# Kernel tuning notes

Hardware: AMD Instinct MI355X
Metric: run time of the kernel (lower is better)

## Reference

```python
import jax, jax.numpy as jnp
import numpy as np
from jax import lax

DIM = 256
HEADS = 8
DIM_HEAD = 32
INNER = HEADS * DIM_HEAD  # 256
FF_MULT = 4
FFI = DIM * FF_MULT       # 1024
TOP_H = 16
TOP_W = 16
EPS_LN = 1e-5
EPS_IN = 1e-5


def conv1x1(x, w, b=None):
    # x: (b,c,h,w), w: (o,c)
    y = jnp.einsum('oc,bchw->bohw', w, x)
    if b is not None:
        y = y + b[None, :, None, None]
    return y


def dwconv3x3(x, w, b):
    # x: (b,c,h,w), w: (c,1,3,3) depthwise
    c = x.shape[1]
    y = lax.conv_general_dilated(x, w, window_strides=(1, 1), padding='SAME',
                                 feature_group_count=c,
                                 dimension_numbers=('NCHW', 'OIHW', 'NCHW'))
    return y + b[None, :, None, None]


def chan_layernorm(x, g, b):
    mean = jnp.mean(x, axis=1, keepdims=True)
    var = jnp.var(x, axis=1, keepdims=True)  # biased, matches unbiased=False
    return (x - mean) / jnp.sqrt(var + EPS_LN) * g + b


def instnorm(x):
    # InstanceNorm2d(affine=False): normalize per (b,c) over spatial dims
    mean = jnp.mean(x, axis=(2, 3), keepdims=True)
    var = jnp.var(x, axis=(2, 3), keepdims=True)
    return (x - mean) / jnp.sqrt(var + EPS_IN)


def l2norm_lastdim(t):
    # F.normalize(t, dim=-1): normalize along the LAST axis (width here)
    n = jnp.sqrt(jnp.sum(t * t, axis=-1, keepdims=True))
    return t / jnp.maximum(n, 1e-12)


def dpsa(x, ln_g, ln_b, w_qkv, w_out, b_out):
    b, c, H, W = x.shape
    xn = chan_layernorm(x, ln_g, ln_b)
    qkv = conv1x1(xn, w_qkv)                       # (b, 3*INNER, H, W)
    q, k, v = jnp.split(qkv, 3, axis=1)
    # fold heads: 'b (h c) x y -> (b h) c x y'
    fold = lambda t: t.reshape(b, HEADS, DIM_HEAD, H, W).reshape(b * HEADS, DIM_HEAD, H, W)
    q, k, v = fold(q), fold(k), fold(v)
    q = l2norm_lastdim(q)
    k = l2norm_lastdim(k)

    B = b * HEADS
    q_probe = jnp.sum(q, axis=(2, 3))              # (B, c)

    # height pruning
    k_height = jnp.sum(k, axis=3)                  # (B, c, H)
    score_r = jnp.einsum('bc,bch->bh', q_probe, k_height)
    _, top_h = lax.top_k(score_r, TOP_H)           # (B, TOP_H)
    idx_h = top_h[:, None, :, None]
    k = jnp.take_along_axis(k, idx_h, axis=2)      # (B, c, TOP_H, W)
    v = jnp.take_along_axis(v, idx_h, axis=2)

    # width pruning
    k_width = jnp.sum(k, axis=2)                   # (B, c, W)
    score_c = jnp.einsum('bc,bcw->bw', q_probe, k_width)
    _, top_w = lax.top_k(score_c, TOP_W)           # (B, TOP_W)
    idx_w = top_w[:, None, None, :]
    k = jnp.take_along_axis(k, idx_w, axis=3)      # (B, c, TOP_H, TOP_W)
    v = jnp.take_along_axis(v, idx_w, axis=3)

    # 'b d h w -> b (h w) d'
    flat = lambda t: t.transpose(0, 2, 3, 1).reshape(B, -1, DIM_HEAD)
    qf, kf, vf = flat(q), flat(k), flat(v)
    sim = jnp.einsum('bid,bjd->bij', qf, kf)       # (B, HW, TOP_H*TOP_W) — no scale, matches source
    attn = jax.nn.softmax(sim, axis=-1)
    out = jnp.einsum('bij,bjd->bid', attn, vf)     # (B, HW, d)
    # '(b h) (x y) d -> b (h d) x y'
    out = out.reshape(b, HEADS, H, W, DIM_HEAD).transpose(0, 1, 4, 2, 3).reshape(b, INNER, H, W)
    return conv1x1(out, w_out, b_out)


def setup_inputs() -> dict:
    key = jax.random.key(0)
    ks = jax.random.split(key, 12)
    s = 0.02
    return {
        'x': jax.random.normal(ks[0], (8, DIM, 64, 64), dtype=jnp.float32),
        'ln_g': jnp.ones((1, DIM, 1, 1), jnp.float32),
        'ln_b': jnp.zeros((1, DIM, 1, 1), jnp.float32),
        'w_qkv': jax.random.normal(ks[1], (3 * INNER, DIM), jnp.float32) * s,
        'w_out': jax.random.normal(ks[2], (DIM, INNER), jnp.float32) * s,
        'b_out': jnp.zeros((DIM,), jnp.float32),
        'w_dw': jax.random.normal(ks[3], (DIM, 1, 3, 3), jnp.float32) * s,
        'b_dw': jnp.zeros((DIM,), jnp.float32),
        'w_comb': jax.random.normal(ks[4], (DIM, 2 * DIM), jnp.float32) * s,
        'b_comb': jnp.zeros((DIM,), jnp.float32),
        'w_ff1': jax.random.normal(ks[5], (FFI, DIM), jnp.float32) * s,
        'b_ff1': jnp.zeros((FFI,), jnp.float32),
        'w_ffdw': jax.random.normal(ks[6], (FFI, 1, 3, 3), jnp.float32) * s,
        'b_ffdw': jnp.zeros((FFI,), jnp.float32),
        'w_ff2': jax.random.normal(ks[7], (DIM, FFI), jnp.float32) * s,
        'b_ff2': jnp.zeros((DIM,), jnp.float32),
    }


def reference(x, ln_g, ln_b, w_qkv, w_out, b_out, w_dw, b_dw, w_comb, b_comb,
              w_ff1, b_ff1, w_ffdw, b_ffdw, w_ff2, b_ff2):
    attn_branch = dpsa(x, ln_g, ln_b, w_qkv, w_out, b_out)
    conv_branch = dwconv3x3(x, w_dw, b_dw)
    combined = jnp.concatenate([attn_branch, conv_branch], axis=1)
    attn_out = conv1x1(combined, w_comb, b_comb) + x
    # feed-forward
    h = conv1x1(attn_out, w_ff1, b_ff1)
    h = jax.nn.gelu(instnorm(h), approximate=False)
    r = jax.nn.gelu(instnorm(dwconv3x3(h, w_ffdw, b_ffdw)), approximate=False)
    h = h + r
    h = conv1x1(h, w_ff2, b_ff2)
    return instnorm(h)
```

## Files before the change

### kernel.cpp

```cpp
#include <hip/hip_runtime.h>
#include <math.h>

constexpr int Bn = 8, Cd = 256, HW = 4096;
constexpr int NPOS = Bn * HW;

typedef __attribute__((ext_vector_type(8))) short bfrag;
typedef __attribute__((ext_vector_type(4))) float facc;
typedef __attribute__((ext_vector_type(8))) unsigned short us8;

static __device__ __forceinline__ float wredsum(float v){
  #pragma unroll
  for (int d=32; d; d>>=1) v += __shfl_xor(v,d,64);
  return v;
}
static __device__ __forceinline__ float gelu_exact(float x){
  return 0.5f*x*(1.f+erff(x*0.70710678118f));
}
static __device__ __forceinline__ unsigned short bf16r(float x){
  unsigned u = __float_as_uint(x);
  u += 0x7FFFu + ((u>>16)&1u);
  return (unsigned short)(u>>16);
}
static __device__ __forceinline__ void split1(float x, unsigned short& h, unsigned short& l){
  unsigned u = __float_as_uint(x);
  unsigned r = (u + 0x7FFFu + ((u>>16)&1u)) & 0xFFFF0000u;
  h = (unsigned short)(r>>16);
  float rest = x - __uint_as_float(r);
  unsigned u2 = __float_as_uint(rest);
  unsigned r2 = u2 + 0x7FFFu + ((u2>>16)&1u);
  l = (unsigned short)(r2>>16);
}

__global__ __launch_bounds__(256) void k_lnsplit(const float* __restrict__ x,
    const float* __restrict__ g, const float* __restrict__ bb,
    unsigned short* __restrict__ xt){
  __shared__ float rs[64][5], rss[64][5];
  int pxi = threadIdx.x & 63;
  int cg  = threadIdx.x >> 6;
  int p = blockIdx.x*64 + pxi;
  int b = p >> 12, pos = p & 4095;
  const float* xb = x + ((size_t)b*Cd + cg*64)*(size_t)HW + pos;
  float s=0.f, ss=0.f;
  #pragma unroll 8
  for (int c=0;c<64;c++){ float v = xb[(size_t)c*HW]; s+=v; ss+=v*v; }
  rs[pxi][cg]=s; rss[pxi][cg]=ss;
  __syncthreads();
  s  = rs[pxi][0]+rs[pxi][1]+rs[pxi][2]+rs[pxi][3];
  ss = rss[pxi][0]+rss[pxi][1]+rss[pxi][2]+rss[pxi][3];
  float mean = s*(1.f/Cd);
  float inv  = rsqrtf(ss*(1.f/Cd) - mean*mean + 1e-5f);
  unsigned short* xh = xt + (size_t)b*2097152ull + (size_t)pos*256u + cg*64;
  unsigned short* xl = xh + 1048576u;
  for (int c0=0;c0<64;c0+=8){
    us8 hv, lv;
    #pragma unroll
    for (int j=0;j<8;j++){
      float v = xb[(size_t)(c0+j)*HW];
      v = (v-mean)*inv*g[cg*64+c0+j] + bb[cg*64+c0+j];
      unsigned short hh,ll; split1(v,hh,ll);
      hv[j]=hh; lv[j]=ll;
    }
    *(us8*)(xh + c0) = hv;
    *(us8*)(xl + c0) = lv;
  }
}

__global__ void k_splitW(const float* __restrict__ w, unsigned short* __restrict__ wh, int n){
  int i = blockIdx.x*256 + threadIdx.x;
  if (i<n){
    unsigned short h,l; split1(w[i],h,l);
    wh[i]=h; wh[n+i]=l;
  }
}
__global__ void k_cvtW(const float* __restrict__ w, unsigned short* __restrict__ wb, int n){
  int i = blockIdx.x*256 + threadIdx.x;
  if (i<n) wb[i] = bf16r(w[i]);
}

__global__ __launch_bounds__(256) void k_mfma3(
    const unsigned short* __restrict__ W2,
    const unsigned short* __restrict__ Xt,
    float* __restrict__ out, int M, int K, long xbs){
  int b  = blockIdx.z;
  int n0 = blockIdx.x*128;
  int m0 = blockIdx.y*128;
  int wave = threadIdx.x>>6, lane = threadIdx.x&63;
  int wm = (wave>>1)*64, wn = (wave&1)*64;
  int l15 = lane&15, half = lane>>4;
  const unsigned short* Wh = W2;
  const unsigned short* Wl = W2 + (size_t)M*K;
  const unsigned short* Xh = Xt + (size_t)b*(size_t)xbs;
  const unsigned short* Xl = Xh + (size_t)4096u*(size_t)K;

  facc acc[4][4];
  #pragma unroll
  for (int i=0;i<4;i++)
    #pragma unroll
    for (int j=0;j<4;j++) acc[i][j] = (facc){0.f,0.f,0.f,0.f};

  const size_t wrow[4] = {
    (size_t)(m0+wm+ 0+l15)*(size_t)K, (size_t)(m0+wm+16+l15)*(size_t)K,
    (size_t)(m0+wm+32+l15)*(size_t)K, (size_t)(m0+wm+48+l15)*(size_t)K };
  const size_t xrow[4] = {
    (size_t)(n0+wn+ 0+l15)*(size_t)K, (size_t)(n0+wn+16+l15)*(size_t)K,
    (size_t)(n0+wn+32+l15)*(size_t)K, (size_t)(n0+wn+48+l15)*(size_t)K };

  for (int k0=0; k0<K; k0+=32){
    int ks = k0 + half*8;
    bfrag ah[4], al[4], bh[4], bl[4];
    #pragma unroll
    for (int i=0;i<4;i++){
      ah[i] = *(const bfrag*)(Wh + wrow[i] + ks);
      al[i] = *(const bfrag*)(Wl + wrow[i] + ks);
      bh[i] = *(const bfrag*)(Xh + xrow[i] + ks);
      bl[i] = *(const bfrag*)(Xl + xrow[i] + ks);
    }
    #pragma unroll
    for (int i=0;i<4;i++)
      #pragma unroll
      for (int j=0;j<4;j++){
        acc[i][j] = __builtin_amdgcn_mfma_f32_16x16x32_bf16(ah[i], bh[j], acc[i][j],0,0,0);
        acc[i][j] = __builtin_amdgcn_mfma_f32_16x16x32_bf16(ah[i], bl[j], acc[i][j],0,0,0);
        acc[i][j] = __builtin_amdgcn_mfma_f32_16x16x32_bf16(al[i], bh[j], acc[i][j],0,0,0);
      }
  }
  #pragma unroll
  for (int i=0;i<4;i++){
    int o = m0+wm+i*16+half*4;
    #pragma unroll
    for (int j=0;j<4;j++){
      int p = n0+wn+j*16+l15;
      size_t ob = ((size_t)b*M + o)*(size_t)HW + p;
      #pragma unroll
      for (int r=0;r<4;r++)
        out[ob + (size_t)r*HW] = acc[i][j][r];
    }
  }
}

template<bool RES>
__global__ __launch_bounds__(256) void k_mfma1(
    const unsigned short* __restrict__ Wb,
    const unsigned short* __restrict__ Xt,
    const float* __restrict__ bias, const float* __restrict__ resid,
    float* __restrict__ out, int M, int K, long xbs){
  int b  = blockIdx.z;
  int n0 = blockIdx.x*128;
  int m0 = blockIdx.y*128;
  int wave = threadIdx.x>>6, lane = threadIdx.x&63;
  int wm = (wave>>1)*64, wn = (wave&1)*64;
  int l15 = lane&15, half = lane>>4;
  const unsigned short* Xh = Xt + (size_t)b*(size_t)xbs;

  facc acc[4][4];
  #pragma unroll
  for (int i=0;i<4;i++)
    #pragma unroll
    for (int j=0;j<4;j++) acc[i][j] = (facc){0.f,0.f,0.f,0.f};

  const size_t wrow[4] = {
    (size_t)(m0+wm+ 0+l15)*(size_t)K, (size_t)(m0+wm+16+l15)*(size_t)K,
    (size_t)(m0+wm+32+l15)*(size_t)K, (size_t)(m0+wm+48+l15)*(size_t)K };
  const size_t xrow[4] = {
    (size_t)(n0+wn+ 0+l15)*(size_t)K, (size_t)(n0+wn+16+l15)*(size_t)K,
    (size_t)(n0+wn+32+l15)*(size_t)K, (size_t)(n0+wn+48+l15)*(size_t)K };

  #pragma unroll 2
  for (int k0=0; k0<K; k0+=32){
    int ks = k0 + half*8;
    bfrag ah[4], bh[4];
    #pragma unroll
    for (int i=0;i<4;i++){
      ah[i] = *(const bfrag*)(Wb + wrow[i] + ks);
      bh[i] = *(const bfrag*)(Xh + xrow[i] + ks);
    }
    #pragma unroll
    for (int i=0;i<4;i++)
      #pragma unroll
      for (int j=0;j<4;j++)
        acc[i][j] = __builtin_amdgcn_mfma_f32_16x16x32_bf16(ah[i], bh[j], acc[i][j],0,0,0);
  }
  #pragma unroll
  for (int i=0;i<4;i++){
    int o = m0+wm+i*16+half*4;
    #pragma unroll
    for (int j=0;j<4;j++){
      int p = n0+wn+j*16+l15;
      size_t ob = ((size_t)b*M + o)*(size_t)HW + p;
      #pragma unroll
      for (int r=0;r<4;r++){
        float v = acc[i][j][r];
        if (bias) v += bias[o+r];
        if (RES)  v += resid[ob + (size_t)r*HW];
        out[ob + (size_t)r*HW] = v;
      }
    }
  }
}

__global__ __launch_bounds__(256) void k_l2norm(float* __restrict__ qkv,
    float* __restrict__ k_height){
  int row  = blockIdx.x*4 + (threadIdx.x>>6);
  int lane = threadIdx.x & 63;
  int part = row >> 17;
  int rem  = row & 131071;
  int Bp   = rem >> 11;
  int c    = (rem >> 6) & 31;
  int h    = rem & 63;
  int b = Bp>>3, hd = Bp&7;
  float* ptr = qkv + ((size_t)b*768 + part*256 + hd*32 + c)*(size_t)HW + h*64;
  float v = ptr[lane];
  float ss = v*v, sv = v;
  #pragma unroll
  for (int d=32; d; d>>=1){ ss += __shfl_xor(ss,d,64); sv += __shfl_xor(sv,d,64); }
  float inv = 1.f / fmaxf(sqrtf(ss), 1e-12f);
  ptr[lane] = v*inv;
  if (lane==0 && part) k_height[(size_t)Bp*2048 + c*64 + h] = sv*inv;
}

__global__ __launch_bounds__(256) void k_qT(const float* __restrict__ qkv,
    unsigned short* __restrict__ qt){
  __shared__ float t[64][33];
  int Bp = blockIdx.y, p0 = blockIdx.x*64;
  int b = Bp>>3, hd = Bp&7;
  const float* qp = qkv + ((size_t)b*768 + hd*32)*(size_t)HW + p0;
  int c8 = threadIdx.x>>6, px = threadIdx.x&63;
  #pragma unroll
  for (int j=0;j<8;j++)
    t[px][c8*8+j] = qp[(size_t)(c8*8+j)*HW + px];
  __syncthreads();
  int px2 = threadIdx.x>>2, ch = threadIdx.x&3;
  us8 hv;
  #pragma unroll
  for (int j=0;j<8;j++) hv[j] = bf16r(t[px2][ch*8+j]);
  *(us8*)(qt + ((size_t)Bp*4096 + p0 + px2)*32 + ch*8) = hv;
}

__global__ __launch_bounds__(256) void k_qprobe(const float* __restrict__ qkv,
    float* __restrict__ q_probe){
  int Bp = blockIdx.x >> 5;
  int c  = blockIdx.x & 31;
  int b = Bp>>3, hd = Bp&7;
  const float* qp = qkv + ((size_t)b*768 + hd*32 + c)*(size_t)HW;
  float s = 0.f;
  for (int i=threadIdx.x*4; i<HW; i+=1024){
    float4 v = *(const float4*)(qp+i);
    s += v.x+v.y+v.z+v.w;
  }
  s = wredsum(s);
  __shared__ float red[4];
  if ((threadIdx.x&63)==0) red[threadIdx.x>>6] = s;
  __syncthreads();
  if (threadIdx.x==0) q_probe[blockIdx.x] = red[0]+red[1]+red[2]+red[3];
}

__global__ void k_score(const float* __restrict__ q_probe,
    const float* __restrict__ agg, float* __restrict__ score){
  int Bp = blockIdx.x; int t = threadIdx.x;
  float s = 0.f;
  for (int c=0;c<32;c++) s += q_probe[Bp*32+c] * agg[(size_t)Bp*2048 + c*64 + t];
  score[Bp*64+t] = s;
}

__global__ void k_topk(const float* __restrict__ score, int* __restrict__ idx){
  int Bp = blockIdx.x; int lane = threadIdx.x;
  float v = score[Bp*64+lane];
  for (int it=0; it<16; ++it){
    float m = v;
    #pragma unroll
    for (int d=32; d; d>>=1) m = fmaxf(m, __shfl_xor(m,d,64));
    unsigned long long mask = __ballot(v==m);
    int sel = __ffsll((unsigned long long)mask) - 1;
    if (lane==0) idx[Bp*16+it] = sel;
    if (lane==sel) v = -3.0e38f;
  }
}

__global__ void k_kwidth(const float* __restrict__ qkv, const int* __restrict__ idx_h,
    float* __restrict__ k_width){
  int c = blockIdx.x, Bp = blockIdx.y, w = threadIdx.x;
  int b = Bp>>3, hd = Bp&7;
  const float* kp = qkv + ((size_t)b*768 + 256 + hd*32 + c)*(size_t)HW;
  float s = 0.f;
  for (int i=0;i<16;i++) s += kp[idx_h[Bp*16+i]*64 + w];
  k_width[(size_t)Bp*2048 + c*64 + w] = s;
}

__global__ __launch_bounds__(256) void k_gather_bf(const float* __restrict__ qkv,
    const int* __restrict__ idx_h, const int* __restrict__ idx_w,
    unsigned short* __restrict__ kfb, unsigned short* __restrict__ vtb){
  int Bp = blockIdx.x; int b = Bp>>3, hd = Bp&7;
  __shared__ int hi[16], wj[16];
  __shared__ int pos_s[256];
  if (threadIdx.x < 16) hi[threadIdx.x] = idx_h[Bp*16+threadIdx.x];
  else if (threadIdx.x < 32) wj[threadIdx.x-16] = idx_w[Bp*16+threadIdx.x-16];
  __syncthreads();
  pos_s[threadIdx.x] = hi[threadIdx.x>>4]*64 + wj[threadIdx.x&15];
  __syncthreads();
  const float* kpl = qkv + ((size_t)b*768 + 256 + hd*32)*(size_t)HW;
  const float* vpl = qkv + ((size_t)b*768 + 512 + hd*32)*(size_t)HW;
  for (int e=threadIdx.x; e<8192; e+=256){
    int t = e>>5, c = e&31;
    kfb[(size_t)Bp*8192 + e] = bf16r(kpl[(size_t)c*HW + pos_s[t]]);
    int c2 = e>>8, t2 = e&255;
    vtb[(size_t)Bp*8192 + e] = bf16r(vpl[(size_t)c2*HW + pos_s[t2]]);
  }
}

__global__ __launch_bounds__(256) void k_attn_mfma(
    const unsigned short* __restrict__ QT,
    const unsigned short* __restrict__ kfb,
    const unsigned short* __restrict__ vtb,
    unsigned short* __restrict__ xout){
  __shared__ unsigned short Pl[4*16*264];
  __shared__ unsigned short obuf[4*16*32];
  __shared__ float lsum[64];
  int Bp = blockIdx.y, qb = blockIdx.x*64;
  int b = Bp>>3, hd = Bp&7;
  int tid = threadIdx.x;
  int wv = tid>>6, lane = tid&63, l15 = lane&15, lq = lane>>4;

  const unsigned short* Kg = kfb + (size_t)Bp*8192;
  const unsigned short* Vg = vtb + (size_t)Bp*8192;

  bfrag aq = *(const bfrag*)(QT + ((size_t)Bp*4096 + qb + wv*16 + l15)*32 + lq*8);

  float ps[4] = {0.f,0.f,0.f,0.f};
  #pragma unroll
  for (int t=0;t<16;t++){
    bfrag bk = *(const bfrag*)(Kg + (t*16+l15)*32 + lq*8);
    facc s = (facc){0.f,0.f,0.f,0.f};
    s = __builtin_amdgcn_mfma_f32_16x16x32_bf16(aq, bk, s, 0,0,0);
    #pragma unroll
    for (int r=0;r<4;r++){
      float pe = __expf(s[r]);
      ps[r] += pe;
      Pl[(wv*16 + lq*4 + r)*264 + t*16 + l15] = bf16r(pe);
    }
  }
  #pragma unroll
  for (int r=0;r<4;r++){
    #pragma unroll
    for (int d=1; d<16; d<<=1) ps[r] += __shfl_xor(ps[r], d, 64);
  }
  if (l15==0){
    #pragma unroll
    for (int r=0;r<4;r++) lsum[wv*16 + lq*4 + r] = ps[r];
  }

  facc o0 = (facc){0.f,0.f,0.f,0.f}, o1 = (facc){0.f,0.f,0.f,0.f};
  #pragma unroll
  for (int ko=0;ko<8;ko++){
    bfrag ap = *(const bfrag*)(Pl + (wv*16 + l15)*264 + ko*32 + lq*8);
    bfrag b0 = *(const bfrag*)(Vg + (l15)*256 + ko*32 + lq*8);
    bfrag b1 = *(const bfrag*)(Vg + (16+l15)*256 + ko*32 + lq*8);
    o0 = __builtin_amdgcn_mfma_f32_16x16x32_bf16(ap, b0, o0, 0,0,0);
    o1 = __builtin_amdgcn_mfma_f32_16x16x32_bf16(ap, b1, o1, 0,0,0);
  }
  #pragma unroll
  for (int r=0;r<4;r++){
    float iv = 1.f / lsum[wv*16 + lq*4 + r];
    obuf[(wv*16 + lq*4 + r)*32 + l15]      = bf16r(o0[r]*iv);
    obuf[(wv*16 + lq*4 + r)*32 + 16 + l15] = bf16r(o1[r]*iv);
  }
  int ql = wv*16 + (lane>>2), ch = lane&3;
  us8 hv = *(const us8*)(obuf + ql*32 + ch*8);
  *(us8*)(xout + (size_t)b*6291456ull + (size_t)(qb + ql)*256u + hd*32 + ch*8) = hv;
}

__global__ __launch_bounds__(256) void k_bf16T(const float* __restrict__ in,
    unsigned short* __restrict__ xt, int Cpart, int Ktot, int coff, int rb0, int wb0){
  int rb = rb0 + blockIdx.z, wb = wb0 + blockIdx.z;
  int c0 = blockIdx.y*64, p0 = blockIdx.x*64;
  __shared__ float t[64][65];
  const float* ip = in + ((size_t)rb*Cpart + c0)*(size_t)HW + p0;
  int tr = threadIdx.x>>4, tc4 = (threadIdx.x&15)*4;
  #pragma unroll
  for (int rr=0; rr<64; rr+=16){
    float4 v = *(const float4*)(ip + (size_t)(tr+rr)*HW + tc4);
    t[tr+rr][tc4+0]=v.x; t[tr+rr][tc4+1]=v.y; t[tr+rr][tc4+2]=v.z; t[tr+rr][tc4+3]=v.w;
  }
  __syncthreads();
  unsigned short* xh = xt + (size_t)wb*4096u*(size_t)Ktot + (size_t)coff + c0;
  #pragma unroll
  for (int rr=0; rr<64; rr+=16){
    int p = tr+rr;
    ushort4 hv;
    hv.x = bf16r(t[tc4+0][p]); hv.y = bf16r(t[tc4+1][p]);
    hv.z = bf16r(t[tc4+2][p]); hv.w = bf16r(t[tc4+3][p]);
    *(ushort4*)(xh + (size_t)(p0+p)*(size_t)Ktot + tc4) = hv;
  }
}

__global__ __launch_bounds__(256) void k_dwbf16(const float* __restrict__ x,
    const float* __restrict__ w, const float* __restrict__ bias,
    unsigned short* __restrict__ xt){
  int p = blockIdx.x*256 + threadIdx.x;
  int b = p >> 12, pos = p & 4095;
  int h = pos>>6, wx = pos&63;
  int c0 = blockIdx.y*64;
  unsigned short* xh = xt + (size_t)b*2097152ull + (size_t)pos*512u + 256u + c0;
  for (int cc=0; cc<64; cc+=8){
    us8 hv;
    #pragma unroll
    for (int j=0;j<8;j++){
      int c = c0+cc+j;
      const float* ip = x + ((size_t)b*Cd + c)*(size_t)HW;
      const float* wp = w + c*9;
      float s = bias[c];
      #pragma unroll
      for (int kh=-1; kh<=1; ++kh){
        int hh = h+kh; if ((unsigned)hh >= 64u) continue;
        #pragma unroll
        for (int kw=-1; kw<=1; ++kw){
          int ww2 = wx+kw; if ((unsigned)ww2 >= 64u) continue;
          s += wp[(kh+1)*3 + (kw+1)] * ip[hh*64 + ww2];
        }
      }
      hv[j] = bf16r(s);
    }
    *(us8*)(xh+cc) = hv;
  }
}

__global__ __launch_bounds__(256) void k_ffn_fused(float* __restrict__ h,
    const float* __restrict__ wdw, const float* __restrict__ bdw){
  __shared__ float lds[4096];
  __shared__ float red[8];
  int plane = blockIdx.x;
  int c = plane & 1023;
  float* hp = h + (size_t)plane*(size_t)HW;
  int t = threadIdx.x;
  int wid = t>>6, lane = t&63;

  float4 v[4];
  float s=0.f, ss=0.f;
  #pragma unroll
  for (int k2=0;k2<4;k2++){
    v[k2] = *(const float4*)(hp + k2*1024 + t*4);
    s  += v[k2].x+v[k2].y+v[k2].z+v[k2].w;
    ss += v[k2].x*v[k2].x+v[k2].y*v[k2].y+v[k2].z*v[k2].z+v[k2].w*v[k2].w;
  }
  s = wredsum(s); ss = wredsum(ss);
  if (lane==0){ red[wid]=s; red[4+wid]=ss; }
  __syncthreads();
  s  = red[0]+red[1]+red[2]+red[3];
  ss = red[4]+red[5]+red[6]+red[7];
  float mean = s*(1.f/HW);
  float inv  = rsqrtf(ss*(1.f/HW) - mean*mean + 1e-5f);

  #pragma unroll
  for (int k2=0;k2<4;k2++){
    int i = k2*1024 + t*4;
    lds[i+0] = gelu_exact((v[k2].x-mean)*inv);
    lds[i+1] = gelu_exact((v[k2].y-mean)*inv);
    lds[i+2] = gelu_exact((v[k2].z-mean)*inv);
    lds[i+3] = gelu_exact((v[k2].w-mean)*inv);
  }
  __syncthreads();

  float w9[9];
  #pragma unroll
  for (int i=0;i<9;i++) w9[i] = wdw[c*9+i];
  float bv = bdw[c];
  float r[16];
  float s2=0.f, ss2=0.f;
  #pragma unroll
  for (int k2=0;k2<4;k2++){
    #pragma unroll
    for (int j=0;j<4;j++){
      int px = k2*1024 + t*4 + j;
      int hh = px>>6, ww = px&63;
      float acc = bv;
      #pragma unroll
      for (int kh=-1; kh<=1; ++kh){
        int h2 = hh+kh; if ((unsigned)h2 >= 64u) continue;
        #pragma unroll
        for (int kw=-1; kw<=1; ++kw){
          int w2 = ww+kw; if ((unsigned)w2 >= 64u) continue;
          acc += w9[(kh+1)*3+(kw+1)] * lds[h2*64 + w2];
        }
      }
      r[k2*4+j] = acc;
      s2 += acc; ss2 += acc*acc;
    }
  }
  s2 = wredsum(s2); ss2 = wredsum(ss2);
  __syncthreads();
  if (lane==0){ red[wid]=s2; red[4+wid]=ss2; }
  __syncthreads();
  s2  = red[0]+red[1]+red[2]+red[3];
  ss2 = red[4]+red[5]+red[6]+red[7];
  float mean2 = s2*(1.f/HW);
  float inv2  = rsqrtf(ss2*(1.f/HW) - mean2*mean2 + 1e-5f);

  #pragma unroll
  for (int k2=0;k2<4;k2++){
    int i = k2*1024 + t*4;
    float4 o;
    o.x = lds[i+0] + gelu_exact((r[k2*4+0]-mean2)*inv2);
    o.y = lds[i+1] + gelu_exact((r[k2*4+1]-mean2)*inv2);
    o.z = lds[i+2] + gelu_exact((r[k2*4+2]-mean2)*inv2);
    o.w = lds[i+3] + gelu_exact((r[k2*4+3]-mean2)*inv2);
    *(float4*)(hp + i) = o;
  }
}

__global__ __launch_bounds__(256) void k_instnorm(const float* __restrict__ in,
    float* __restrict__ out){
  size_t base = (size_t)blockIdx.x * HW;
  const float* p = in + base;
  float s=0.f, ss=0.f;
  for (int i=threadIdx.x*4; i<HW; i+=1024){
    float4 v = *(const float4*)(p+i);
    s  += v.x+v.y+v.z+v.w;
    ss += v.x*v.x+v.y*v.y+v.z*v.z+v.w*v.w;
  }
  s = wredsum(s); ss = wredsum(ss);
  __shared__ float sh[8];
  int wid = threadIdx.x>>6;
  if ((threadIdx.x&63)==0){ sh[wid]=s; sh[4+wid]=ss; }
  __syncthreads();
  s  = sh[0]+sh[1]+sh[2]+sh[3];
  ss = sh[4]+sh[5]+sh[6]+sh[7];
  float mean = s*(1.f/HW);
  float inv  = rsqrtf(ss*(1.f/HW) - mean*mean + 1e-5f);
  for (int i=threadIdx.x*4; i<HW; i+=1024){
    float4 v = *(const float4*)(p+i);
    float4 r;
    r.x = (v.x-mean)*inv; r.y = (v.y-mean)*inv; r.z = (v.z-mean)*inv; r.w = (v.w-mean)*inv;
    *(float4*)(out + base + i) = r;
  }
}

extern "C" void kernel_launch(void* const* d_in, const int* in_sizes, int n_in,
                              void* d_out, int out_size, void* d_ws, size_t ws_size,
                              hipStream_t stream){
  const float* x      = (const float*)d_in[0];
  const float* ln_g   = (const float*)d_in[1];
  const float* ln_bb  = (const float*)d_in[2];
  const float* w_qkv  = (const float*)d_in[3];
  const float* w_out  = (const float*)d_in[4];
  const float* b_out  = (const float*)d_in[5];
  const float* w_dw   = (const float*)d_in[6];
  const float* b_dw   = (const float*)d_in[7];
  const float* w_comb = (const float*)d_in[8];
  const float* b_comb = (const float*)d_in[9];
  const float* w_ff1  = (const float*)d_in[10];
  const float* b_ff1  = (const float*)d_in[11];
  const float* w_ffdw = (const float*)d_in[12];
  const float* b_ffdw = (const float*)d_in[13];
  const float* w_ff2  = (const float*)d_in[14];
  const float* b_ff2  = (const float*)d_in[15];
  float* out = (float*)d_out;
  float* ws  = (float*)d_ws;

  float* A    = ws;
  float* Q    = ws + 8388608ull;
  float* Hb   = ws + 8388608ull;
  float* F2o  = ws + 8388608ull;
  unsigned short* XT2 = (unsigned short*)(ws + 16777216ull);
  unsigned short* XTa = (unsigned short*)(ws + 33554432ull);
  unsigned short* QT  = (unsigned short*)(ws + 33554432ull);
  unsigned short* KFB = (unsigned short*)(ws + 37748736ull);
  unsigned short* VTB = (unsigned short*)(ws + 38010880ull);
  unsigned short* Xattn = (unsigned short*)(Q + 2097152ull);
  unsigned short* XT3a = (unsigned short*)ws;
  unsigned short* XT3b = (unsigned short*)d_out;
  unsigned short* XTb  = (unsigned short*)d_out;
  float* S = ws;
  float* k_height = S;
  float* k_width  = S + 131072;
  float* q_probe  = S + 262144;
  float* score_r  = S + 264192;
  float* score_c  = S + 268288;
  int*   idx_h    = (int*)(S + 272384);
  int*   idx_w    = idx_h + 1024;
  unsigned short* W2qkv = (unsigned short*)(ws + 41943040ull);
  unsigned short* Wb_out  = W2qkv + 393216;
  unsigned short* Wb_comb = Wb_out + 65536;
  unsigned short* Wb_ff1  = Wb_comb + 131072;
  unsigned short* Wb_ff2  = Wb_ff1 + 262144;

  k_splitW<<<(196608+255)/256, 256, 0, stream>>>(w_qkv, W2qkv, 196608);
  k_cvtW<<<(65536 +255)/256, 256, 0, stream>>>(w_out,  Wb_out,  65536);
  k_cvtW<<<(131072+255)/256, 256, 0, stream>>>(w_comb, Wb_comb, 131072);
  k_cvtW<<<(262144+255)/256, 256, 0, stream>>>(w_ff1,  Wb_ff1, 262144);
  k_cvtW<<<(262144+255)/256, 256, 0, stream>>>(w_ff2,  Wb_ff2, 262144);

  k_lnsplit<<<512, 256, 0, stream>>>(x, ln_g, ln_bb, XTa);
  k_mfma3<<<dim3(32,6,8), 256, 0, stream>>>(W2qkv, XTa, Q, 768, 256, 2097152);
  k_l2norm<<<65536, 256, 0, stream>>>(Q, k_height);
  k_qT<<<dim3(64,64), 256, 0, stream>>>(Q, QT);
  k_qprobe<<<2048, 256, 0, stream>>>(Q, q_probe);
  k_score<<<64, 64, 0, stream>>>(q_probe, k_height, score_r);
  k_topk<<<64, 64, 0, stream>>>(score_r, idx_h);
  k_kwidth<<<dim3(32,64), 64, 0, stream>>>(Q, idx_h, k_width);
  k_score<<<64, 64, 0, stream>>>(q_probe, k_width, score_c);
  k_topk<<<64, 64, 0, stream>>>(score_c, idx_w);
  k_gather_bf<<<64, 256, 0, stream>>>(Q, idx_h, idx_w, KFB, VTB);
  k_attn_mfma<<<dim3(64,64), 256, 0, stream>>>(QT, KFB, VTB, Xattn);
  k_mfma1<false><<<dim3(32,2,8), 256, 0, stream>>>(Wb_out, Xattn, b_out, nullptr, (float*)d_out, 256, 256, 6291456);

  k_bf16T<<<dim3(64,4,8), 256, 0, stream>>>((const float*)d_out, XT2, 256, 512, 0, 0, 0);
  k_dwbf16<<<dim3(128,4), 256, 0, stream>>>(x, w_dw, b_dw, XT2);
  k_mfma1<true><<<dim3(32,2,8), 256, 0, stream>>>(Wb_comb, XT2, b_comb, x, A, 256, 512, 2097152);

  k_bf16T<<<dim3(64,4,8), 256, 0, stream>>>(A, XTb, 256, 256, 0, 0, 0);
  k_mfma1<false><<<dim3(32,8,8), 256, 0, stream>>>(Wb_ff1, XTb, b_ff1, nullptr, Hb, 1024, 256, 1048576);
  k_ffn_fused<<<Bn*1024, 256, 0, stream>>>(Hb, w_ffdw, b_ffdw);
  k_bf16T<<<dim3(64,16,4), 256, 0, stream>>>(Hb, XT3a, 1024, 1024, 0, 0, 0);
  k_bf16T<<<dim3(64,16,4), 256, 0, stream>>>(Hb, XT3b, 1024, 1024, 0, 4, 0);
  k_mfma1<false><<<dim3(32,2,4), 256, 0, stream>>>(Wb_ff2, XT3a, b_ff2, nullptr, F2o, 256, 1024, 4194304);
  k_mfma1<false><<<dim3(32,2,4), 256, 0, stream>>>(Wb_ff2, XT3b, b_ff2, nullptr, F2o + 4ull*256*HW, 256, 1024, 4194304);
  k_instnorm<<<Bn*256, 256, 0, stream>>>(F2o, (float*)d_out);
}
```

Baseline: 864.8 us.

## Coalesce transposed bf16 stores via LDS and fuse q_probe into l2norm

Result: faster. 813.1 us (-6.0%).

```diff
diff --git a/kernel.cpp b/kernel.cpp
--- a/kernel.cpp
+++ b/kernel.cpp
@@ -35,10 +35,13 @@
     const float* __restrict__ g, const float* __restrict__ bb,
     unsigned short* __restrict__ xt){
   __shared__ float rs[64][5], rss[64][5];
-  int pxi = threadIdx.x & 63;
-  int cg  = threadIdx.x >> 6;
+  __shared__ unsigned short lt[64*262];
+  int tid = threadIdx.x;
+  int pxi = tid & 63;
+  int cg  = tid >> 6;
   int p = blockIdx.x*64 + pxi;
   int b = p >> 12, pos = p & 4095;
+  int pos0 = (blockIdx.x*64) & 4095;
   const float* xb = x + ((size_t)b*Cd + cg*64)*(size_t)HW + pos;
   float s=0.f, ss=0.f;
   #pragma unroll 8
@@ -49,19 +52,44 @@
   ss = rss[pxi][0]+rss[pxi][1]+rss[pxi][2]+rss[pxi][3];
   float mean = s*(1.f/Cd);
   float inv  = rsqrtf(ss*(1.f/Cd) - mean*mean + 1e-5f);
-  unsigned short* xh = xt + (size_t)b*2097152ull + (size_t)pos*256u + cg*64;
-  unsigned short* xl = xh + 1048576u;
+
+  us8 lv_r[8];
+  #pragma unroll
   for (int c0=0;c0<64;c0+=8){
-    us8 hv, lv;
     #pragma unroll
     for (int j=0;j<8;j++){
       float v = xb[(size_t)(c0+j)*HW];
       v = (v-mean)*inv*g[cg*64+c0+j] + bb[cg*64+c0+j];
       unsigned short hh,ll; split1(v,hh,ll);
-      hv[j]=hh; lv[j]=ll;
-    }
-    *(us8*)(xh + c0) = hv;
-    *(us8*)(xl + c0) = lv;
+      lt[pxi*262 + cg*64 + c0 + j] = hh;
+      lv_r[c0>>3][j] = ll;
+    }
+  }
+  __syncthreads();
+  unsigned short* xp = xt + (size_t)b*2097152ull + (size_t)pos0*256u;
+  #pragma unroll
+  for (int i=0;i<8;i++){
+    int e = i*256 + tid;
+    int pl = e>>5, ch = e&31;
+    us8 hv;
+    #pragma unroll
+    for (int j=0;j<8;j++) hv[j] = lt[pl*262 + ch*8 + j];
+    *(us8*)(xp + (size_t)pl*256u + ch*8) = hv;
+  }
+  __syncthreads();
+  #pragma unroll
+  for (int c0=0;c0<64;c0+=8)
+    #pragma unroll
+    for (int j=0;j<8;j++) lt[pxi*262 + cg*64 + c0 + j] = lv_r[c0>>3][j];
+  __syncthreads();
+  #pragma unroll
+  for (int i=0;i<8;i++){
+    int e = i*256 + tid;
+    int pl = e>>5, ch = e&31;
+    us8 hv;
+    #pragma unroll
+    for (int j=0;j<8;j++) hv[j] = lt[pl*262 + ch*8 + j];
+    *(us8*)(xp + 1048576u + (size_t)pl*256u + ch*8) = hv;
   }
 }
 
@@ -199,23 +227,40 @@
 }
 
 __global__ __launch_bounds__(256) void k_l2norm(float* __restrict__ qkv,
-    float* __restrict__ k_height){
-  int row  = blockIdx.x*4 + (threadIdx.x>>6);
-  int lane = threadIdx.x & 63;
+    float* __restrict__ k_height, float* __restrict__ qrow){
+  int row = blockIdx.x*16 + (threadIdx.x>>4);
+  int l16 = threadIdx.x & 15;
   int part = row >> 17;
   int rem  = row & 131071;
   int Bp   = rem >> 11;
   int c    = (rem >> 6) & 31;
   int h    = rem & 63;
   int b = Bp>>3, hd = Bp&7;
-  float* ptr = qkv + ((size_t)b*768 + part*256 + hd*32 + c)*(size_t)HW + h*64;
-  float v = ptr[lane];
-  float ss = v*v, sv = v;
-  #pragma unroll
-  for (int d=32; d; d>>=1){ ss += __shfl_xor(ss,d,64); sv += __shfl_xor(sv,d,64); }
+  float* ptr = qkv + ((size_t)b*768 + part*256 + hd*32 + c)*(size_t)HW + h*64 + l16*4;
+  float4 v = *(const float4*)ptr;
+  float ss = v.x*v.x+v.y*v.y+v.z*v.z+v.w*v.w;
+  float sv = v.x+v.y+v.z+v.w;
+  #pragma unroll
+  for (int d=1; d<16; d<<=1){ ss += __shfl_xor(ss,d,64); sv += __shfl_xor(sv,d,64); }
   float inv = 1.f / fmaxf(sqrtf(ss), 1e-12f);
-  ptr[lane] = v*inv;
-  if (lane==0 && part) k_height[(size_t)Bp*2048 + c*64 + h] = sv*inv;
+  v.x*=inv; v.y*=inv; v.z*=inv; v.w*=inv;
+  *(float4*)ptr = v;
+  if (l16==0){
+    float rsum = sv*inv;
+    if (part) k_height[(size_t)Bp*2048 + c*64 + h] = rsum;
+    else      qrow[(size_t)Bp*2048 + c*64 + h] = rsum;
+  }
+}
+
+__global__ void k_qprobe2(const float* __restrict__ qrow, float* __restrict__ q_probe){
+  int Bp = blockIdx.x; int t = threadIdx.x;
+  int c = t>>3, h0 = (t&7)*8;
+  float s = 0.f;
+  #pragma unroll
+  for (int j=0;j<8;j++) s += qrow[(size_t)Bp*2048 + c*64 + h0 + j];
+  #pragma unroll
+  for (int d=1; d<8; d<<=1) s += __shfl_xor(s,d,64);
+  if ((t&7)==0) q_probe[Bp*32+c] = s;
 }
 
 __global__ __launch_bounds__(256) void k_qT(const float* __restrict__ qkv,
@@ -234,24 +279,6 @@
   #pragma unroll
   for (int j=0;j<8;j++) hv[j] = bf16r(t[px2][ch*8+j]);
   *(us8*)(qt + ((size_t)Bp*4096 + p0 + px2)*32 + ch*8) = hv;
-}
-
-__global__ __launch_bounds__(256) void k_qprobe(const float* __restrict__ qkv,
-    float* __restrict__ q_probe){
-  int Bp = blockIdx.x >> 5;
-  int c  = blockIdx.x & 31;
-  int b = Bp>>3, hd = Bp&7;
-  const float* qp = qkv + ((size_t)b*768 + hd*32 + c)*(size_t)HW;
-  float s = 0.f;
-  for (int i=threadIdx.x*4; i<HW; i+=1024){
-    float4 v = *(const float4*)(qp+i);
-    s += v.x+v.y+v.z+v.w;
-  }
-  s = wredsum(s);
-  __shared__ float red[4];
-  if ((threadIdx.x&63)==0) red[threadIdx.x>>6] = s;
-  __syncthreads();
-  if (threadIdx.x==0) q_probe[blockIdx.x] = red[0]+red[1]+red[2]+red[3];
 }
 
 __global__ void k_score(const float* __restrict__ q_probe,
@@ -382,44 +409,52 @@
   }
   __syncthreads();
   unsigned short* xh = xt + (size_t)wb*4096u*(size_t)Ktot + (size_t)coff + c0;
-  #pragma unroll
-  for (int rr=0; rr<64; rr+=16){
-    int p = tr+rr;
-    ushort4 hv;
-    hv.x = bf16r(t[tc4+0][p]); hv.y = bf16r(t[tc4+1][p]);
-    hv.z = bf16r(t[tc4+2][p]); hv.w = bf16r(t[tc4+3][p]);
-    *(ushort4*)(xh + (size_t)(p0+p)*(size_t)Ktot + tc4) = hv;
+  int chunk = threadIdx.x & 7;
+  #pragma unroll
+  for (int i=0;i<2;i++){
+    int pix = (threadIdx.x>>3) + 32*i;
+    us8 hv;
+    #pragma unroll
+    for (int j=0;j<8;j++) hv[j] = bf16r(t[chunk*8+j][pix]);
+    *(us8*)(xh + (size_t)(p0+pix)*(size_t)Ktot + chunk*8) = hv;
   }
 }
 
 __global__ __launch_bounds__(256) void k_dwbf16(const float* __restrict__ x,
     const float* __restrict__ w, const float* __restrict__ bias,
     unsigned short* __restrict__ xt){
-  int p = blockIdx.x*256 + threadIdx.x;
+  __shared__ unsigned short lt[256*65];
+  int tid = threadIdx.x;
+  int p = blockIdx.x*256 + tid;
   int b = p >> 12, pos = p & 4095;
+  int pos0 = (blockIdx.x*256) & 4095;
   int h = pos>>6, wx = pos&63;
   int c0 = blockIdx.y*64;
-  unsigned short* xh = xt + (size_t)b*2097152ull + (size_t)pos*512u + 256u + c0;
-  for (int cc=0; cc<64; cc+=8){
+  for (int cc=0; cc<64; cc++){
+    int c = c0+cc;
+    const float* ip = x + ((size_t)b*Cd + c)*(size_t)HW;
+    const float* wp = w + c*9;
+    float s = bias[c];
+    #pragma unroll
+    for (int kh=-1; kh<=1; ++kh){
+      int hh = h+kh; if ((unsigned)hh >= 64u) continue;
+      #pragma unroll
+      for (int kw=-1; kw<=1; ++kw){
+        int ww2 = wx+kw; if ((unsigned)ww2 >= 64u) continue;
+        s += wp[(kh+1)*3 + (kw+1)] * ip[hh*64 + ww2];
+      }
+    }
+    lt[tid*65 + cc] = bf16r(s);
+  }
+  __syncthreads();
+  int chunk = tid & 7;
+  #pragma unroll
+  for (int i=0;i<8;i++){
+    int row = (tid>>3) + 32*i;
     us8 hv;
     #pragma unroll
-    for (int j=0;j<8;j++){
-      int c = c0+cc+j;
-      const float* ip = x + ((size_t)b*Cd + c)*(size_t)HW;
-      const float* wp = w + c*9;
-      float s = bias[c];
-      #pragma unroll
-      for (int kh=-1; kh<=1; ++kh){
-        int hh = h+kh; if ((unsigned)hh >= 64u) continue;
-        #pragma unroll
-        for (int kw=-1; kw<=1; ++kw){
-          int ww2 = wx+kw; if ((unsigned)ww2 >= 64u) continue;
-          s += wp[(kh+1)*3 + (kw+1)] * ip[hh*64 + ww2];
-        }
-      }
-      hv[j] = bf16r(s);
-    }
-    *(us8*)(xh+cc) = hv;
+    for (int j=0;j<8;j++) hv[j] = lt[row*65 + chunk*8 + j];
+    *(us8*)(xt + (size_t)b*2097152ull + (size_t)(pos0+row)*512u + 256u + c0 + chunk*8) = hv;
   }
 }
 
@@ -571,10 +606,11 @@
   float* S = ws;
   float* k_height = S;
   float* k_width  = S + 131072;
-  float* q_probe  = S + 262144;
-  float* score_r  = S + 264192;
-  float* score_c  = S + 268288;
-  int*   idx_h    = (int*)(S + 272384);
+  float* qrow     = S + 262144;
+  float* q_probe  = S + 393216;
+  float* score_r  = S + 395264;
+  float* score_c  = S + 399360;
+  int*   idx_h    = (int*)(S + 403456);
   int*   idx_w    = idx_h + 1024;
   unsigned short* W2qkv = (unsigned short*)(ws + 41943040ull);
   unsigned short* Wb_out  = W2qkv + 393216;
@@ -590,9 +626,9 @@
 
   k_lnsplit<<<512, 256, 0, stream>>>(x, ln_g, ln_bb, XTa);
   k_mfma3<<<dim3(32,6,8), 256, 0, stream>>>(W2qkv, XTa, Q, 768, 256, 2097152);
-  k_l2norm<<<65536, 256, 0, stream>>>(Q, k_height);
+  k_l2norm<<<16384, 256, 0, stream>>>(Q, k_height, qrow);
+  k_qprobe2<<<64, 256, 0, stream>>>(qrow, q_probe);
   k_qT<<<dim3(64,64), 256, 0, stream>>>(Q, QT);
-  k_qprobe<<<2048, 256, 0, stream>>>(Q, q_probe);
   k_score<<<64, 64, 0, stream>>>(q_probe, k_height, score_r);
   k_topk<<<64, 64, 0, stream>>>(score_r, idx_h);
   k_kwidth<<<dim3(32,64), 64, 0, stream>>>(Q, idx_h, k_width);
```
